# Optimization experiments

Hardware: AMD Instinct MI355X
Metric: run time of the kernel (lower is better)

Reference implementation:

```python
import jax, jax.numpy as jnp
import numpy as np

LAMBDA_GEO = 0.5


def setup_inputs() -> dict:
    key = jax.random.key(0)
    embeddings = jax.random.normal(key, (4, 2048, 512), dtype=jnp.float32)
    return {"embeddings": embeddings}


def _geometric_loss(embeddings):
    b, s, d = embeddings.shape
    x = embeddings.reshape(b * s, d)  # [N, d]
    sq_norm = jnp.sum(x * x, axis=-1)  # [N]
    sq = sq_norm[:, None] + sq_norm[None, :] - 2.0 * (x @ x.T)  # [N, N]
    sq = jnp.maximum(sq, 0.0)
    dist = jnp.sqrt(sq)  # torch.cdist(p=2)
    return jnp.mean(jnp.exp(-dist * 0.1)) * 0.1


def reference(embeddings):
    geometric_loss = _geometric_loss(embeddings)
    total_geometric = LAMBDA_GEO * geometric_loss
    return geometric_loss, total_geometric
```

## Files before the change

kernel.cpp:

```cpp
#include <hip/hip_runtime.h>

#define NROWS 8192
#define DIM   512
#define NT    64
#define NTRI  (NT * (NT + 1) / 2)
#define NACC  64

using f32x4 = __attribute__((ext_vector_type(4))) float;

typedef __attribute__((address_space(1))) const void* as1_cvptr;
typedef __attribute__((address_space(3))) void*       as3_vptr;

__device__ __forceinline__ void async16(const void* g, void* l) {
    __builtin_amdgcn_global_load_lds((as1_cvptr)g, (as3_vptr)l, 16, 0, 0);
}

__device__ __forceinline__ unsigned char f2e4m3(float x) {
    unsigned ux = __float_as_uint(x);
    unsigned s  = (ux >> 24) & 0x80u;
    float a = __uint_as_float(ux & 0x7FFFFFFFu);
    a = fminf(a, 448.0f);
    unsigned ua = __float_as_uint(a);
    int eb = (int)(ua >> 23);
    if (eb < 121) eb = 121;
    float step  = __uint_as_float((unsigned)(eb - 3) << 23);
    float istep = __uint_as_float((unsigned)(257 - eb) << 23);
    float q = rintf(a * istep) * step;
    q = fminf(q, 448.0f);
    if (q < 0.001953125f)
        return (unsigned char)s;
    unsigned uq = __float_as_uint(q);
    int eq = (int)(uq >> 23) - 127;
    unsigned byte;
    if (eq < -6) byte = (unsigned)(q * 512.0f);
    else         byte = (unsigned)((eq + 7) << 3) | ((uq >> 20) & 7u);
    return (unsigned char)(s | byte);
}

__global__ __launch_bounds__(256) void norm_convert_kernel(
    const float* __restrict__ X, unsigned char* __restrict__ Xq,
    float* __restrict__ norms, float* __restrict__ acc)
{
    const int tid  = threadIdx.x;
    const int lane = tid & 63;
    const int w    = tid >> 6;
    const int row  = blockIdx.x * 4 + w;

    if (blockIdx.x == 0 && tid < NACC) acc[tid] = 0.0f;

    const float* xr = X + (size_t)row * DIM + lane * 8;
    float4 v0 = *(const float4*)xr;
    float4 v1 = *(const float4*)(xr + 4);

    float s = 0.0f;
    s = fmaf(v0.x, v0.x, s); s = fmaf(v0.y, v0.y, s);
    s = fmaf(v0.z, v0.z, s); s = fmaf(v0.w, v0.w, s);
    s = fmaf(v1.x, v1.x, s); s = fmaf(v1.y, v1.y, s);
    s = fmaf(v1.z, v1.z, s); s = fmaf(v1.w, v1.w, s);

    union { unsigned char b[8]; uint2 v; } pk;
    pk.b[0] = f2e4m3(v0.x); pk.b[1] = f2e4m3(v0.y);
    pk.b[2] = f2e4m3(v0.z); pk.b[3] = f2e4m3(v0.w);
    pk.b[4] = f2e4m3(v1.x); pk.b[5] = f2e4m3(v1.y);
    pk.b[6] = f2e4m3(v1.z); pk.b[7] = f2e4m3(v1.w);

    const int h    = lane >> 5;
    const int cs   = lane & 31;
    const int cpos = cs ^ (row & 15);
    *(uint2*)(Xq + (size_t)row * DIM + h * 256 + cpos * 8) = pk.v;

    #pragma unroll
    for (int off = 32; off > 0; off >>= 1) s += __shfl_down(s, off, 64);
    if (lane == 0) norms[row] = s;
}

__global__ __launch_bounds__(256, 2) void pair_loss_gemm_kernel(
    const unsigned char* __restrict__ Xq, const float* __restrict__ norms,
    float* __restrict__ acc)
{
    __shared__ __align__(16) char As[32768];
    __shared__ __align__(16) char Bs[32768];
    __shared__ float wsum[4];

    int t = blockIdx.x, bi = 0;
    while (t >= (NT - bi)) { t -= (NT - bi); bi++; }
    const int bj = bi + t;

    const int tid  = threadIdx.x;
    const int lane = tid & 63;
    const int w    = tid >> 6;

    const int rowA = bi * 128;
    const int rowB = bj * 128;

    f32x4 accv[4][4];
    const f32x4 zero = {0.0f, 0.0f, 0.0f, 0.0f};
    #pragma unroll
    for (int a = 0; a < 4; a++)
        #pragma unroll
        for (int b = 0; b < 4; b++) accv[a][b] = zero;

    const int rl = lane >> 4;
    const int pc = lane & 15;
    const unsigned char* gA = Xq + (size_t)(rowA + rl) * DIM + pc * 16;
    const unsigned char* gB = Xq + (size_t)(rowB + rl) * DIM + pc * 16;

    const int fr = lane & 15;
    const int q  = lane >> 4;
    const int wr = (w & 1) * 64;
    const int wc = (w >> 1) * 64;

    #pragma unroll 1
    for (int h = 0; h < 2; h++) {
        #pragma unroll
        for (int n = 0; n < 8; n++) {
            const int go = h * 256 + (w * 8 + n) * 2048;
            const int lo = (w * 8 + n) * 1024;
            async16(gA + go, As + lo);
            async16(gB + go, Bs + lo);
        }
        __syncthreads();

        #pragma unroll
        for (int s = 0; s < 8; s++) {
            const int off = (((s * 4 + q) ^ fr) & 31) * 8;
            long af[4], bf[4];
            #pragma unroll
            for (int a = 0; a < 4; a++)
                af[a] = *(const long*)(As + (wr + a * 16 + fr) * 256 + off);
            #pragma unroll
            for (int b = 0; b < 4; b++)
                bf[b] = *(const long*)(Bs + (wc + b * 16 + fr) * 256 + off);
            #pragma unroll
            for (int a = 0; a < 4; a++)
                #pragma unroll
                for (int b = 0; b < 4; b++)
                    accv[a][b] = __builtin_amdgcn_mfma_f32_16x16x32_fp8_fp8(
                        af[a], bf[b], accv[a][b], 0, 0, 0);
        }
        if (h == 0) __syncthreads();
    }

    const float wgt = (bi == bj) ? 1.0f : 2.0f;
    float lsum = 0.0f;
    #pragma unroll
    for (int a = 0; a < 4; a++) {
        const int gi0 = rowA + wr + a * 16 + (lane >> 4) * 4;
        #pragma unroll
        for (int b = 0; b < 4; b++) {
            const int gj = rowB + wc + b * 16 + (lane & 15);
            const float nj = norms[gj];
            #pragma unroll
            for (int r = 0; r < 4; r++) {
                const int gi = gi0 + r;
                float sq = fmaf(-2.0f, accv[a][b][r], norms[gi] + nj);
                sq = fmaxf(sq, 0.0f);
                float term = __expf(-0.1f * sqrtf(sq));
                if (gi == gj) term = 1.0f;
                lsum += term;
            }
        }
    }
    lsum *= wgt;
    #pragma unroll
    for (int off = 32; off > 0; off >>= 1) lsum += __shfl_down(lsum, off, 64);
    if (lane == 0) wsum[w] = lsum;
    __syncthreads();
    if (tid == 0)
        atomicAdd(&acc[blockIdx.x & (NACC - 1)],
                  wsum[0] + wsum[1] + wsum[2] + wsum[3]);
}

__global__ void finalize_kernel(const float* __restrict__ acc,
                                float* __restrict__ out)
{
    const int lane = threadIdx.x;
    float s = (lane < NACC) ? acc[lane] : 0.0f;
    #pragma unroll
    for (int off = 32; off > 0; off >>= 1) s += __shfl_down(s, off, 64);
    if (lane == 0) {
        const float inv = 1.0f / ((float)NROWS * (float)NROWS);
        float loss = s * inv * 0.1f;
        out[0] = loss;
        out[1] = 0.5f * loss;
    }
}

extern "C" void kernel_launch(void* const* d_in, const int* in_sizes, int n_in,
                              void* d_out, int out_size, void* d_ws, size_t ws_size,
                              hipStream_t stream)
{
    const float* X = (const float*)d_in[0];
    float* out = (float*)d_out;

    char* ws = (char*)d_ws;
    float*         acc   = (float*)ws;
    float*         norms = (float*)(ws + 1024);
    unsigned char* Xq    = (unsigned char*)(ws + 1024 + 32768);

    norm_convert_kernel<<<NROWS / 4, 256, 0, stream>>>(X, Xq, norms, acc);
    pair_loss_gemm_kernel<<<NTRI, 256, 0, stream>>>(Xq, norms, acc);
    finalize_kernel<<<1, 64, 0, stream>>>(acc, out);
}
```

Measured before the change: 114.2 us.

## Use gfx950 scaled 16x16x128 FP8 MFMA with double-buffered 128-wide K tiles

Replaces the 16x16x32 fp8 MFMA with the gfx950 scaled 16x16x128 f8f6f4 instruction, using unit scales, so each instruction covers four times the K depth. The K loop is restructured into four 128-byte chunks with double-buffered LDS, and the next chunk's async loads are issued before the current MFMAs to overlap load with compute. The global fp8 layout and LDS swizzle change to 16-byte granules XORed by row so that each 32-byte fragment can be read as two uint4 loads. This adds barriers per chunk and depends on the swizzle matching between producer and consumer.

```diff
diff --git a/kernel.cpp b/kernel.cpp
--- a/kernel.cpp
+++ b/kernel.cpp
@@ -7,6 +7,7 @@
 #define NACC  64
 
 using f32x4 = __attribute__((ext_vector_type(4))) float;
+using i32x8 = __attribute__((ext_vector_type(8))) int;
 
 typedef __attribute__((address_space(1))) const void* as1_cvptr;
 typedef __attribute__((address_space(3))) void*       as3_vptr;
@@ -64,10 +65,11 @@
     pk.b[4] = f2e4m3(v1.x); pk.b[5] = f2e4m3(v1.y);
     pk.b[6] = f2e4m3(v1.z); pk.b[7] = f2e4m3(v1.w);
 
-    const int h    = lane >> 5;
-    const int cs   = lane & 31;
-    const int cpos = cs ^ (row & 15);
-    *(uint2*)(Xq + (size_t)row * DIM + h * 256 + cpos * 8) = pk.v;
+    const int g    = lane >> 4;
+    const int p    = (lane & 15) >> 1;
+    const int h    = lane & 1;
+    const int ppos = p ^ (row & 7);
+    *(uint2*)(Xq + (size_t)row * DIM + g * 128 + ppos * 16 + h * 8) = pk.v;
 
     #pragma unroll
     for (int off = 32; off > 0; off >>= 1) s += __shfl_down(s, off, 64);
@@ -78,8 +80,8 @@
     const unsigned char* __restrict__ Xq, const float* __restrict__ norms,
     float* __restrict__ acc)
 {
-    __shared__ __align__(16) char As[32768];
-    __shared__ __align__(16) char Bs[32768];
+    __shared__ __align__(16) char As[2][16384];
+    __shared__ __align__(16) char Bs[2][16384];
     __shared__ float wsum[4];
 
     int t = blockIdx.x, bi = 0;
@@ -100,45 +102,66 @@
         #pragma unroll
         for (int b = 0; b < 4; b++) accv[a][b] = zero;
 
-    const int rl = lane >> 4;
-    const int pc = lane & 15;
-    const unsigned char* gA = Xq + (size_t)(rowA + rl) * DIM + pc * 16;
-    const unsigned char* gB = Xq + (size_t)(rowB + rl) * DIM + pc * 16;
-
-    const int fr = lane & 15;
-    const int q  = lane >> 4;
-    const int wr = (w & 1) * 64;
-    const int wc = (w >> 1) * 64;
+    const unsigned char* gA =
+        Xq + (size_t)(rowA + w * 32 + (lane >> 3)) * DIM + (lane & 7) * 16;
+    const unsigned char* gB =
+        Xq + (size_t)(rowB + w * 32 + (lane >> 3)) * DIM + (lane & 7) * 16;
+    const int ldw = w * 4096;
+
+    const int fr  = lane & 15;
+    const int q   = lane >> 4;
+    const int foL = ((2 * q)     ^ (fr & 7)) * 16;
+    const int foH = ((2 * q + 1) ^ (fr & 7)) * 16;
+    const int wr  = (w & 1) * 64;
+    const int wc  = (w >> 1) * 64;
+
+    #pragma unroll
+    for (int n = 0; n < 4; n++) {
+        async16(gA + n * 4096, As[0] + ldw + n * 1024);
+        async16(gB + n * 4096, Bs[0] + ldw + n * 1024);
+    }
+    __syncthreads();
 
     #pragma unroll 1
-    for (int h = 0; h < 2; h++) {
-        #pragma unroll
-        for (int n = 0; n < 8; n++) {
-            const int go = h * 256 + (w * 8 + n) * 2048;
-            const int lo = (w * 8 + n) * 1024;
-            async16(gA + go, As + lo);
-            async16(gB + go, Bs + lo);
-        }
-        __syncthreads();
-
-        #pragma unroll
-        for (int s = 0; s < 8; s++) {
-            const int off = (((s * 4 + q) ^ fr) & 31) * 8;
-            long af[4], bf[4];
+    for (int g = 0; g < 4; g++) {
+        const int cur = g & 1;
+        const char* curA = As[cur];
+        const char* curB = Bs[cur];
+
+        union { uint4 h[2]; i32x8 v; } af[4], bf[4];
+        #pragma unroll
+        for (int a = 0; a < 4; a++) {
+            const char* rb = curA + (wr + a * 16 + fr) * 128;
+            af[a].h[0] = *(const uint4*)(rb + foL);
+            af[a].h[1] = *(const uint4*)(rb + foH);
+        }
+        #pragma unroll
+        for (int b = 0; b < 4; b++) {
+            const char* rb = curB + (wc + b * 16 + fr) * 128;
+            bf[b].h[0] = *(const uint4*)(rb + foL);
+            bf[b].h[1] = *(const uint4*)(rb + foH);
+        }
+
+        const bool more = (g < 3);
+        if (more) {
+            const int nxt = cur ^ 1;
+            const int go  = (g + 1) * 128;
             #pragma unroll
-            for (int a = 0; a < 4; a++)
-                af[a] = *(const long*)(As + (wr + a * 16 + fr) * 256 + off);
+            for (int n = 0; n < 4; n++) {
+                async16(gA + go + n * 4096, As[nxt] + ldw + n * 1024);
+                async16(gB + go + n * 4096, Bs[nxt] + ldw + n * 1024);
+            }
+        }
+
+        #pragma unroll
+        for (int a = 0; a < 4; a++)
             #pragma unroll
             for (int b = 0; b < 4; b++)
-                bf[b] = *(const long*)(Bs + (wc + b * 16 + fr) * 256 + off);
-            #pragma unroll
-            for (int a = 0; a < 4; a++)
-                #pragma unroll
-                for (int b = 0; b < 4; b++)
-                    accv[a][b] = __builtin_amdgcn_mfma_f32_16x16x32_fp8_fp8(
-                        af[a], bf[b], accv[a][b], 0, 0, 0);
-        }
-        if (h == 0) __syncthreads();
+                accv[a][b] = __builtin_amdgcn_mfma_scale_f32_16x16x128_f8f6f4(
+                    af[a].v, bf[b].v, accv[a][b], 0, 0,
+                    0, 0x7F7F7F7F, 0, 0x7F7F7F7F);
+
+        if (more) __syncthreads();
     }
 
     const float wgt = (bi == bj) ? 1.0f : 2.0f;
```

After: 111.4 us. 1.03x faster.
